# Kernel optimization log

Hardware: AMD Instinct MI355X
Metric: run time of the kernel (lower is better)

## Reference

```python
import jax, jax.numpy as jnp
import numpy as np

HQ, HKV, D = 16, 2, 128   # num_heads_q, num_heads_kv, head_dim
G = HQ // HKV             # q heads per kv head (repeat_interleave factor)


def setup_inputs() -> dict:
    key = jax.random.key(0)
    ks = jax.random.split(key, 6)
    B, T, C = 2, 2048, 2048
    def w(k, shape):
        return jax.random.normal(k, shape, jnp.float32) * (1.0 / np.sqrt(shape[0]).astype(np.float32))
    x = jax.random.normal(ks[0], (B, T, C), jnp.float32)
    Wq = w(ks[1], (C, HQ * D))
    Wk = w(ks[2], (C, HKV * D))
    Wv = w(ks[3], (C, HKV * D))
    Wo = w(ks[4], (HQ * D, C))
    Wg = w(ks[5], (C, HQ))
    # causal mask: True where attention is disallowed (j > i)
    mask = jnp.triu(jnp.ones((T, T), dtype=bool), k=1)[None, None]  # (1,1,T,T)
    return {"x": x, "mask": mask, "Wq": Wq, "Wk": Wk, "Wv": Wv, "Wo": Wo, "Wg": Wg}


def reference(x, mask, Wq, Wk, Wv, Wo, Wg):
    B, T, C = x.shape
    # repeat_interleave(G, dim=heads) means q head h uses kv head h // G,
    # so group q heads as (HKV, G) instead of materializing repeated K/V.
    q = (x @ Wq).reshape(B, T, HKV, G, D).transpose(0, 2, 3, 1, 4)  # (B,HKV,G,T,D)
    k = (x @ Wk).reshape(B, T, HKV, D).transpose(0, 2, 1, 3)        # (B,HKV,T,D)
    v = (x @ Wv).reshape(B, T, HKV, D).transpose(0, 2, 1, 3)        # (B,HKV,T,D)
    scale = jnp.float32(1.0 / np.sqrt(D))
    scores = jnp.einsum('bkgtd,bksd->bkgts', q, k) * scale          # (B,HKV,G,T,T)
    scores = jnp.where(mask[:, None], jnp.float32(-1e9), scores)    # causal fill
    attn = jax.nn.softmax(scores, axis=-1)
    # post-softmax sigmoid gate, one scalar per (batch, q-head, query token)
    gates = jax.nn.sigmoid(x @ Wg)                                   # (B,T,HQ)
    gates = gates.transpose(0, 2, 1).reshape(B, HKV, G, T)           # (B,HKV,G,T)
    out = jnp.einsum('bkgts,bksd->btkgd', attn * gates[..., None], v)
    out = out.reshape(B, T, HQ * D)
    return out @ Wo
```

## Files before the change

### kernel.cpp

```cpp
#include <hip/hip_runtime.h>
#include <hip/hip_bf16.h>
#include <math.h>

#define HQ 16
#define HKV 2
#define D 128
#define B_SZ 2
#define T_SZ 2048
#define C_SZ 2048
#define QKVN 2688

#define C_Q 0.12753102f
#define C_G 1.44269504f

typedef __attribute__((ext_vector_type(8))) short short8;
typedef __attribute__((ext_vector_type(4))) float floatx4;

static __device__ __forceinline__ float fexp2(float x) {
    return __builtin_amdgcn_exp2f(x);
}

static __device__ __forceinline__ unsigned short f2b(float f) {
    union { float f; unsigned u; } x; x.f = f;
    return (unsigned short)((x.u + 0x7fffu + ((x.u >> 16) & 1u)) >> 16);
}

static __device__ __forceinline__ unsigned int pk2(float a, float b) {
    float2 t; t.x = a; t.y = b;
    __hip_bfloat162 h = __float22bfloat162_rn(t);
    return *(unsigned int*)&h;
}

static __device__ __forceinline__ void load_lds16(const void* g, void* l) {
    __builtin_amdgcn_global_load_lds(
        (const __attribute__((address_space(1))) void*)g,
        (__attribute__((address_space(3))) void*)l,
        16, 0, 0);
}

static __device__ __forceinline__ void tr32(
    const float* __restrict__ in, unsigned short* __restrict__ out,
    int R, int Cc, float premul, int bx, int by, float (*t)[33])
{
    const int bc = bx * 32, br = by * 32;
    const int tid = threadIdx.x;
    const int r = tid >> 3, c4 = (tid & 7) * 4;
    float4 v = *(const float4*)(in + (size_t)(br + r) * Cc + bc + c4);
    t[r][c4 + 0] = v.x; t[r][c4 + 1] = v.y; t[r][c4 + 2] = v.z; t[r][c4 + 3] = v.w;
    __syncthreads();
    ushort4 o;
    o.x = f2b(t[c4 + 0][r] * premul); o.y = f2b(t[c4 + 1][r] * premul);
    o.z = f2b(t[c4 + 2][r] * premul); o.w = f2b(t[c4 + 3][r] * premul);
    *(ushort4*)(out + (size_t)(bc + r) * R + br + c4) = o;
}

__global__ __launch_bounds__(256) void prep_kernel(
    const float* __restrict__ x,  const float* __restrict__ Wq,
    const float* __restrict__ Wk, const float* __restrict__ Wv,
    const float* __restrict__ Wo, const float* __restrict__ Wg,
    unsigned short* __restrict__ xb, unsigned short* __restrict__ Wqkvt,
    unsigned short* __restrict__ Wot)
{
    __shared__ float t[32][33];
    const int bid = blockIdx.x;
    const int tid = threadIdx.x;
    if (bid < 4096) {
        int i = bid * 2048 + tid * 8;
        float4 a = *(const float4*)(x + i);
        float4 b = *(const float4*)(x + i + 4);
        ushort4 o0, o1;
        o0.x = f2b(a.x); o0.y = f2b(a.y); o0.z = f2b(a.z); o0.w = f2b(a.w);
        o1.x = f2b(b.x); o1.y = f2b(b.y); o1.z = f2b(b.z); o1.w = f2b(b.w);
        *(ushort4*)(xb + i) = o0;
        *(ushort4*)(xb + i + 4) = o1;
    } else if (bid < 8192) {
        int n = bid - 4096;
        tr32(Wq, Wqkvt, C_SZ, HQ * D, C_Q, n & 63, n >> 6, t);
    } else if (bid < 8704) {
        int n = bid - 8192;
        tr32(Wk, Wqkvt + (size_t)(HQ * D) * C_SZ, C_SZ, HKV * D, 1.0f, n & 7, n >> 3, t);
    } else if (bid < 9216) {
        int n = bid - 8704;
        tr32(Wv, Wqkvt + (size_t)(HQ * D + HKV * D) * C_SZ, C_SZ, HKV * D, 1.0f, n & 7, n >> 3, t);
    } else if (bid < 13312) {
        int n = bid - 9216;
        tr32(Wo, Wot, HQ * D, C_SZ, 1.0f, n & 63, n >> 6, t);
    } else {
        int k = (bid - 13312) * 256 + tid;
        const float4* wr = (const float4*)(Wg + (size_t)k * 16);
        float4 w0 = wr[0], w1 = wr[1], w2 = wr[2], w3 = wr[3];
        float w[16] = {w0.x, w0.y, w0.z, w0.w, w1.x, w1.y, w1.z, w1.w,
                       w2.x, w2.y, w2.z, w2.w, w3.x, w3.y, w3.z, w3.w};
        unsigned short* out = Wqkvt + (size_t)(HQ * D + 2 * HKV * D) * C_SZ;
        #pragma unroll
        for (int h = 0; h < 16; ++h)
            out[(size_t)h * C_SZ + k] = f2b(w[h] * C_G);
    }
}

__global__ __launch_bounds__(256) void gemm_bt_bf16(
    const unsigned short* __restrict__ A, const unsigned short* __restrict__ Bt,
    float* __restrict__ Cf, unsigned short* __restrict__ Cb,
    unsigned short* __restrict__ Vt, int M, int N, int K, int out_bf16)
{
    __shared__ __align__(16) unsigned short SM[8448];
    unsigned short* As = SM;
    unsigned short* Bs = SM + 4096;
    const int tid = threadIdx.x;
    const int lane = tid & 63, wave = tid >> 6;
    const int l15 = lane & 15, quad = lane >> 4;
    const int wr = wave >> 1, wc = wave & 1;
    const int bm = blockIdx.y * 128, bn = blockIdx.x * 128;

    floatx4 zero = {0.f, 0.f, 0.f, 0.f};
    floatx4 acc[4][4];
    #pragma unroll
    for (int i = 0; i < 4; ++i)
        #pragma unroll
        for (int j = 0; j < 4; ++j) acc[i][j] = zero;

    int arow[2], acol[2];
    #pragma unroll
    for (int it = 0; it < 2; ++it) {
        int idx = it * 256 + tid;
        int row = idx >> 2, sb = idx & 3;
        int cb = sb ^ ((row >> 1) & 3);
        arow[it] = row; acol[it] = cb * 8;
    }
    const int sw = quad ^ ((l15 >> 1) & 3);

    for (int k0 = 0; k0 < K; k0 += 32) {
        __syncthreads();
        #pragma unroll
        for (int it = 0; it < 2; ++it) {
            load_lds16(A  + (size_t)(bm + arow[it]) * K + k0 + acol[it],
                       &As[(it * 256 + wave * 64) * 8]);
            load_lds16(Bt + (size_t)(bn + arow[it]) * K + k0 + acol[it],
                       &Bs[(it * 256 + wave * 64) * 8]);
        }
        __syncthreads();

        short8 af[4], bf[4];
        #pragma unroll
        for (int mt = 0; mt < 4; ++mt)
            af[mt] = *(const short8*)&As[((wr * 64 + mt * 16 + l15) * 4 + sw) * 8];
        #pragma unroll
        for (int nt = 0; nt < 4; ++nt)
            bf[nt] = *(const short8*)&Bs[((wc * 64 + nt * 16 + l15) * 4 + sw) * 8];
        #pragma unroll
        for (int mt = 0; mt < 4; ++mt)
            #pragma unroll
            for (int nt = 0; nt < 4; ++nt)
                acc[mt][nt] = __builtin_amdgcn_mfma_f32_16x16x32_bf16(
                    af[mt], bf[nt], acc[mt][nt], 0, 0, 0);
    }

    if (Vt && (bn == 2304 || bn == 2432)) {
        unsigned short (*Ct)[132] = (unsigned short(*)[132])SM;
        const int bb = bm >> 11;
        const int tl = bm & 2047;
        #pragma unroll
        for (int vn = 0; vn < 2; ++vn) {
            __syncthreads();
            if (wc == vn) {
                #pragma unroll
                for (int mt = 0; mt < 4; ++mt)
                    #pragma unroll
                    for (int nt = 0; nt < 4; ++nt)
                        #pragma unroll
                        for (int r = 0; r < 4; ++r)
                            Ct[nt * 16 + l15][wr * 64 + mt * 16 + quad * 4 + r] =
                                f2b(acc[mt][nt][r]);
            }
            __syncthreads();
            int row = tid >> 2, cs = (tid & 3) * 32;
            int vrow = (bn - 2304) + vn * 64 + row;
            unsigned short* dst = Vt + ((size_t)bb * (HKV * D) + vrow) * T_SZ + tl + cs;
            const unsigned short* src = &Ct[row][cs];
            short8 v0 = *(const short8*)(src + 0);
            short8 v1 = *(const short8*)(src + 8);
            short8 v2 = *(const short8*)(src + 16);
            short8 v3 = *(const short8*)(src + 24);
            *(short8*)(dst + 0)  = v0; *(short8*)(dst + 8)  = v1;
            *(short8*)(dst + 16) = v2; *(short8*)(dst + 24) = v3;
        }
        return;
    }

    #pragma unroll
    for (int mt = 0; mt < 4; ++mt)
        #pragma unroll
        for (int nt = 0; nt < 4; ++nt)
            #pragma unroll
            for (int r = 0; r < 4; ++r) {
                int m = bm + wr * 64 + mt * 16 + quad * 4 + r;
                int n = bn + wc * 64 + nt * 16 + l15;
                if (out_bf16) Cb[(size_t)m * N + n] = f2b(acc[mt][nt][r]);
                else          Cf[(size_t)m * N + n] = acc[mt][nt][r];
            }
}

__global__ __launch_bounds__(256) void attn_mfma(
    const unsigned short* __restrict__ QKV, const unsigned short* __restrict__ Vt,
    unsigned short* __restrict__ Ob)
{
    __shared__ __align__(16) unsigned short SMEM[64 * 128 + 128 * 64 + 4 * 16 * 72];
    unsigned short* Ks = SMEM;
    unsigned short* Vs = SMEM + 64 * 128;
    unsigned short* Ps = SMEM + 64 * 128 + 128 * 64;
    unsigned short* Lo = SMEM;

    const int bh = blockIdx.x;
    const int qt = (int)gridDim.y - 1 - (int)blockIdx.y;
    const int b = bh >> 4, h = bh & 15, kvh = h >> 3;
    const int tid = threadIdx.x;
    const int lane = tid & 63, w = tid >> 6;
    const int l15 = lane & 15, quad = lane >> 4;
    const int q_local = w * 16 + l15;
    const float BIAS = 32.0f;

    short8 aq[4];
    {
        const unsigned short* qp = QKV + (size_t)(b * T_SZ + qt * 64 + q_local) * QKVN
                                       + h * D + quad * 8;
        #pragma unroll
        for (int kd = 0; kd < 4; ++kd) aq[kd] = *(const short8*)(qp + kd * 32);
    }

    const unsigned short* kg[4];
    const unsigned short* vg[4];
    #pragma unroll
    for (int it = 0; it < 4; ++it) {
        int Bi = it * 256 + tid;
        int kr = Bi >> 4, kc = ((Bi & 15) ^ (kr & 15)) * 8;
        kg[it] = QKV + (size_t)(b * T_SZ + kr) * QKVN + HQ * D + kvh * D + kc;
        int vr = Bi >> 3, vc = ((Bi & 7) ^ (vr & 7)) * 8;
        vg[it] = Vt + (size_t)((b * HKV + kvh) * D + vr) * T_SZ + vc;
    }

    floatx4 zero = {0.f, 0.f, 0.f, 0.f};
    floatx4 oacc[8];
    #pragma unroll
    for (int dt = 0; dt < 8; ++dt) oacc[dt] = zero;
    float l_part = 0.f;

    for (int kt = 0; kt <= qt; ++kt) {
        __syncthreads();
        #pragma unroll
        for (int it = 0; it < 4; ++it) {
            load_lds16(kg[it] + (size_t)kt * 64 * QKVN, &Ks[(it * 256 + w * 64) * 8]);
            load_lds16(vg[it] + kt * 64,                &Vs[(it * 256 + w * 64) * 8]);
        }
        __syncthreads();

        floatx4 sacc[4];
        #pragma unroll
        for (int nt = 0; nt < 4; ++nt) sacc[nt] = zero;
        #pragma unroll
        for (int kd = 0; kd < 4; ++kd)
            #pragma unroll
            for (int nt = 0; nt < 4; ++nt) {
                short8 ak = *(const short8*)&Ks[((nt * 16 + l15) * 16 + ((kd * 4 + quad) ^ l15)) * 8];
                sacc[nt] = __builtin_amdgcn_mfma_f32_16x16x32_bf16(ak, aq[kd], sacc[nt], 0, 0, 0);
            }

        float p[4][4];
        if (kt == qt) {
            #pragma unroll
            for (int nt = 0; nt < 4; ++nt)
                #pragma unroll
                for (int r = 0; r < 4; ++r) {
                    float e = fexp2(sacc[nt][r] - BIAS);
                    p[nt][r] = (nt * 16 + quad * 4 + r > q_local) ? 0.f : e;
                }
        } else {
            #pragma unroll
            for (int nt = 0; nt < 4; ++nt)
                #pragma unroll
                for (int r = 0; r < 4; ++r)
                    p[nt][r] = fexp2(sacc[nt][r] - BIAS);
        }
        #pragma unroll
        for (int nt = 0; nt < 4; ++nt) {
            l_part += (p[nt][0] + p[nt][1]) + (p[nt][2] + p[nt][3]);
            uint2 pw;
            pw.x = pk2(p[nt][0], p[nt][1]);
            pw.y = pk2(p[nt][2], p[nt][3]);
            *(uint2*)&Ps[(w * 16 + l15) * 72 + nt * 16 + quad * 4] = pw;
        }

        #pragma unroll
        for (int kk = 0; kk < 2; ++kk) {
            short8 bp = *(const short8*)&Ps[(w * 16 + l15) * 72 + kk * 32 + quad * 8];
            #pragma unroll
            for (int dt = 0; dt < 8; ++dt) {
                short8 av = *(const short8*)&Vs[((dt * 16 + l15) * 8 + ((kk * 4 + quad) ^ (l15 & 7))) * 8];
                oacc[dt] = __builtin_amdgcn_mfma_f32_16x16x32_bf16(av, bp, oacc[dt], 0, 0, 0);
            }
        }
    }

    float l = l_part;
    l += __shfl_xor(l, 16);
    l += __shfl_xor(l, 32);

    __syncthreads();
    {
        int token = b * T_SZ + qt * 64 + q_local;
        unsigned short gl = QKV[(size_t)token * QKVN + HQ * D + HKV * D * 2 + h];
        union { unsigned u; float f; } gx; gx.u = ((unsigned)gl) << 16;
        float g = 1.0f / (1.0f + fexp2(-gx.f));
        float f = g / l;
        #pragma unroll
        for (int dt = 0; dt < 8; ++dt) {
            uint2 ov;
            ov.x = pk2(oacc[dt][0] * f, oacc[dt][1] * f);
            ov.y = pk2(oacc[dt][2] * f, oacc[dt][3] * f);
            *(uint2*)&Lo[(size_t)q_local * 136 + dt * 16 + quad * 4] = ov;
        }
    }
    __syncthreads();
    {
        int row = tid >> 2, c0 = (tid & 3) * 32;
        size_t tok = (size_t)(b * T_SZ + qt * 64 + row);
        unsigned short* op = Ob + tok * (HQ * D) + h * D + c0;
        const unsigned short* lp = &Lo[(size_t)row * 136 + c0];
        short8 v0 = *(const short8*)(lp + 0);
        short8 v1 = *(const short8*)(lp + 8);
        short8 v2 = *(const short8*)(lp + 16);
        short8 v3 = *(const short8*)(lp + 24);
        *(short8*)(op + 0)  = v0; *(short8*)(op + 8)  = v1;
        *(short8*)(op + 16) = v2; *(short8*)(op + 24) = v3;
    }
}

extern "C" void kernel_launch(void* const* d_in, const int* in_sizes, int n_in,
                              void* d_out, int out_size, void* d_ws, size_t ws_size,
                              hipStream_t stream) {
    const float* x  = (const float*)d_in[0];
    const float* Wq = (const float*)d_in[2];
    const float* Wk = (const float*)d_in[3];
    const float* Wv = (const float*)d_in[4];
    const float* Wo = (const float*)d_in[5];
    const float* Wg = (const float*)d_in[6];
    float* out = (float*)d_out;

    const size_t KB = 1ull << 10;
    char* p = (char*)d_ws;
    unsigned short* xb    = (unsigned short*)(p);
    unsigned short* Ob    = xb;
    unsigned short* Wqkvt = (unsigned short*)(p + 16384 * KB);
    unsigned short* Wot   = (unsigned short*)(p + 27136 * KB);
    unsigned short* QKV   = (unsigned short*)(p + 35328 * KB);
    unsigned short* Vt    = (unsigned short*)(p + 56832 * KB);
    const int BT = B_SZ * T_SZ;

    prep_kernel<<<dim3(13320), 256, 0, stream>>>(x, Wq, Wk, Wv, Wo, Wg, xb, Wqkvt, Wot);

    gemm_bt_bf16<<<dim3(QKVN / 128, BT / 128), 256, 0, stream>>>(
        xb, Wqkvt, nullptr, QKV, Vt, BT, QKVN, C_SZ, 1);

    attn_mfma<<<dim3(B_SZ * HQ, T_SZ / 64), 256, 0, stream>>>(QKV, Vt, Ob);

    gemm_bt_bf16<<<dim3(C_SZ / 128, BT / 128), 256, 0, stream>>>(
        Ob, Wot, out, nullptr, nullptr, BT, C_SZ, HQ * D, 0);
}
```

Measured before the change: 314.2 us.

## Use 32x32x16 MFMA and 128-query tiles in attention kernel

The attention kernel now processes 128 query rows per block (32 per wave) instead of 64, and switches from 16x16x32 to 32x32x16 bf16 MFMA instructions for both QK^T and PV. Each K/V tile loaded into LDS is therefore reused across twice as many queries, and the larger MFMA reduces LDS fragment reads per flop. The epilogue writes output in two passes through LDS. In exchange, register pressure rises, the grid has half as many blocks, and causal blocks waste more work on masked tiles.

After: 325.2 us. +3.5%, slower.

```diff
diff --git a/kernel.cpp b/kernel.cpp
--- a/kernel.cpp
+++ b/kernel.cpp
@@ -15,6 +15,7 @@
 
 typedef __attribute__((ext_vector_type(8))) short short8;
 typedef __attribute__((ext_vector_type(4))) float floatx4;
+typedef __attribute__((ext_vector_type(16))) float floatx16;
 
 static __device__ __forceinline__ float fexp2(float x) {
     return __builtin_amdgcn_exp2f(x);
@@ -204,10 +205,10 @@
     const unsigned short* __restrict__ QKV, const unsigned short* __restrict__ Vt,
     unsigned short* __restrict__ Ob)
 {
-    __shared__ __align__(16) unsigned short SMEM[64 * 128 + 128 * 64 + 4 * 16 * 72];
+    __shared__ __align__(16) unsigned short SMEM[8192 + 8192 + 4 * 32 * 72];
     unsigned short* Ks = SMEM;
-    unsigned short* Vs = SMEM + 64 * 128;
-    unsigned short* Ps = SMEM + 64 * 128 + 128 * 64;
+    unsigned short* Vs = SMEM + 8192;
+    unsigned short* Ps = SMEM + 16384;
     unsigned short* Lo = SMEM;
 
     const int bh = blockIdx.x;
@@ -215,16 +216,17 @@
     const int b = bh >> 4, h = bh & 15, kvh = h >> 3;
     const int tid = threadIdx.x;
     const int lane = tid & 63, w = tid >> 6;
-    const int l15 = lane & 15, quad = lane >> 4;
-    const int q_local = w * 16 + l15;
+    const int l31 = lane & 31, hi = lane >> 5;
+    const int q_local = w * 32 + l31;
+    const int qglob_l = qt * 128 + q_local;
     const float BIAS = 32.0f;
 
-    short8 aq[4];
+    short8 aq[8];
     {
-        const unsigned short* qp = QKV + (size_t)(b * T_SZ + qt * 64 + q_local) * QKVN
-                                       + h * D + quad * 8;
-        #pragma unroll
-        for (int kd = 0; kd < 4; ++kd) aq[kd] = *(const short8*)(qp + kd * 32);
+        const unsigned short* qp = QKV + (size_t)(b * T_SZ + qglob_l) * QKVN
+                                       + h * D + hi * 8;
+        #pragma unroll
+        for (int kd = 0; kd < 8; ++kd) aq[kd] = *(const short8*)(qp + kd * 16);
     }
 
     const unsigned short* kg[4];
@@ -238,13 +240,15 @@
         vg[it] = Vt + (size_t)((b * HKV + kvh) * D + vr) * T_SZ + vc;
     }
 
-    floatx4 zero = {0.f, 0.f, 0.f, 0.f};
-    floatx4 oacc[8];
-    #pragma unroll
-    for (int dt = 0; dt < 8; ++dt) oacc[dt] = zero;
+    floatx16 oacc[4];
+    #pragma unroll
+    for (int dt2 = 0; dt2 < 4; ++dt2)
+        #pragma unroll
+        for (int r = 0; r < 16; ++r) oacc[dt2][r] = 0.f;
     float l_part = 0.f;
 
-    for (int kt = 0; kt <= qt; ++kt) {
+    const int ktmax = 2 * qt + 1;
+    for (int kt = 0; kt <= ktmax; ++kt) {
         __syncthreads();
         #pragma unroll
         for (int it = 0; it < 4; ++it) {
@@ -253,76 +257,84 @@
         }
         __syncthreads();
 
-        floatx4 sacc[4];
-        #pragma unroll
-        for (int nt = 0; nt < 4; ++nt) sacc[nt] = zero;
-        #pragma unroll
-        for (int kd = 0; kd < 4; ++kd)
-            #pragma unroll
-            for (int nt = 0; nt < 4; ++nt) {
-                short8 ak = *(const short8*)&Ks[((nt * 16 + l15) * 16 + ((kd * 4 + quad) ^ l15)) * 8];
-                sacc[nt] = __builtin_amdgcn_mfma_f32_16x16x32_bf16(ak, aq[kd], sacc[nt], 0, 0, 0);
-            }
-
-        float p[4][4];
-        if (kt == qt) {
-            #pragma unroll
-            for (int nt = 0; nt < 4; ++nt)
+        floatx16 sacc[2];
+        #pragma unroll
+        for (int kt2 = 0; kt2 < 2; ++kt2)
+            #pragma unroll
+            for (int r = 0; r < 16; ++r) sacc[kt2][r] = 0.f;
+        #pragma unroll
+        for (int kd = 0; kd < 8; ++kd)
+            #pragma unroll
+            for (int kt2 = 0; kt2 < 2; ++kt2) {
+                short8 ak = *(const short8*)&Ks[((kt2 * 32 + l31) * 16
+                                + ((kd * 2 + hi) ^ (l31 & 15))) * 8];
+                sacc[kt2] = __builtin_amdgcn_mfma_f32_32x32x16_bf16(
+                    ak, aq[kd], sacc[kt2], 0, 0, 0);
+            }
+
+        #pragma unroll
+        for (int kt2 = 0; kt2 < 2; ++kt2) {
+            float p[16];
+            #pragma unroll
+            for (int r = 0; r < 16; ++r) p[r] = fexp2(sacc[kt2][r] - BIAS);
+            if (kt >= 2 * qt) {
                 #pragma unroll
-                for (int r = 0; r < 4; ++r) {
-                    float e = fexp2(sacc[nt][r] - BIAS);
-                    p[nt][r] = (nt * 16 + quad * 4 + r > q_local) ? 0.f : e;
+                for (int r = 0; r < 16; ++r) {
+                    int key = kt * 64 + kt2 * 32 + (r & 3) + 4 * hi + 8 * (r >> 2);
+                    if (key > qglob_l) p[r] = 0.f;
                 }
-        } else {
-            #pragma unroll
-            for (int nt = 0; nt < 4; ++nt)
+            }
+            #pragma unroll
+            for (int g = 0; g < 4; ++g) {
+                l_part += (p[4 * g] + p[4 * g + 1]) + (p[4 * g + 2] + p[4 * g + 3]);
+                uint2 pw;
+                pw.x = pk2(p[4 * g], p[4 * g + 1]);
+                pw.y = pk2(p[4 * g + 2], p[4 * g + 3]);
+                *(uint2*)&Ps[(w * 32 + l31) * 72 + kt2 * 32 + 8 * g + 4 * hi] = pw;
+            }
+        }
+
+        #pragma unroll
+        for (int kk = 0; kk < 4; ++kk) {
+            short8 bp = *(const short8*)&Ps[(w * 32 + l31) * 72 + kk * 16 + hi * 8];
+            #pragma unroll
+            for (int dt2 = 0; dt2 < 4; ++dt2) {
+                short8 av = *(const short8*)&Vs[((dt2 * 32 + l31) * 8
+                                + ((kk * 2 + hi) ^ (l31 & 7))) * 8];
+                oacc[dt2] = __builtin_amdgcn_mfma_f32_32x32x16_bf16(
+                    av, bp, oacc[dt2], 0, 0, 0);
+            }
+        }
+    }
+
+    float l = l_part + __shfl_xor(l_part, 32);
+
+    float f;
+    {
+        unsigned short gl = QKV[(size_t)(b * T_SZ + qglob_l) * QKVN + HQ * D + 2 * HKV * D + h];
+        union { unsigned u; float ff; } gx; gx.u = ((unsigned)gl) << 16;
+        float g = 1.0f / (1.0f + fexp2(-gx.ff));
+        f = g / l;
+    }
+
+    #pragma unroll
+    for (int pass = 0; pass < 2; ++pass) {
+        __syncthreads();
+        if ((w >> 1) == pass) {
+            int lr = (w & 1) * 32 + l31;
+            #pragma unroll
+            for (int dt2 = 0; dt2 < 4; ++dt2)
                 #pragma unroll
-                for (int r = 0; r < 4; ++r)
-                    p[nt][r] = fexp2(sacc[nt][r] - BIAS);
-        }
-        #pragma unroll
-        for (int nt = 0; nt < 4; ++nt) {
-            l_part += (p[nt][0] + p[nt][1]) + (p[nt][2] + p[nt][3]);
-            uint2 pw;
-            pw.x = pk2(p[nt][0], p[nt][1]);
-            pw.y = pk2(p[nt][2], p[nt][3]);
-            *(uint2*)&Ps[(w * 16 + l15) * 72 + nt * 16 + quad * 4] = pw;
-        }
-
-        #pragma unroll
-        for (int kk = 0; kk < 2; ++kk) {
-            short8 bp = *(const short8*)&Ps[(w * 16 + l15) * 72 + kk * 32 + quad * 8];
-            #pragma unroll
-            for (int dt = 0; dt < 8; ++dt) {
-                short8 av = *(const short8*)&Vs[((dt * 16 + l15) * 8 + ((kk * 4 + quad) ^ (l15 & 7))) * 8];
-                oacc[dt] = __builtin_amdgcn_mfma_f32_16x16x32_bf16(av, bp, oacc[dt], 0, 0, 0);
-            }
-        }
-    }
-
-    float l = l_part;
-    l += __shfl_xor(l, 16);
-    l += __shfl_xor(l, 32);
-
-    __syncthreads();
-    {
-        int token = b * T_SZ + qt * 64 + q_local;
-        unsigned short gl = QKV[(size_t)token * QKVN + HQ * D + HKV * D * 2 + h];
-        union { unsigned u; float f; } gx; gx.u = ((unsigned)gl) << 16;
-        float g = 1.0f / (1.0f + fexp2(-gx.f));
-        float f = g / l;
-        #pragma unroll
-        for (int dt = 0; dt < 8; ++dt) {
-            uint2 ov;
-            ov.x = pk2(oacc[dt][0] * f, oacc[dt][1] * f);
-            ov.y = pk2(oacc[dt][2] * f, oacc[dt][3] * f);
-            *(uint2*)&Lo[(size_t)q_local * 136 + dt * 16 + quad * 4] = ov;
-        }
-    }
-    __syncthreads();
-    {
+                for (int g = 0; g < 4; ++g) {
+                    uint2 ov;
+                    ov.x = pk2(oacc[dt2][4 * g + 0] * f, oacc[dt2][4 * g + 1] * f);
+                    ov.y = pk2(oacc[dt2][4 * g + 2] * f, oacc[dt2][4 * g + 3] * f);
+                    *(uint2*)&Lo[lr * 136 + dt2 * 32 + 8 * g + 4 * hi] = ov;
+                }
+        }
+        __syncthreads();
         int row = tid >> 2, c0 = (tid & 3) * 32;
-        size_t tok = (size_t)(b * T_SZ + qt * 64 + row);
+        size_t tok = (size_t)(b * T_SZ + qt * 128 + pass * 64 + row);
         unsigned short* op = Ob + tok * (HQ * D) + h * D + c0;
         const unsigned short* lp = &Lo[(size_t)row * 136 + c0];
         short8 v0 = *(const short8*)(lp + 0);
@@ -360,7 +372,7 @@
     gemm_bt_bf16<<<dim3(QKVN / 128, BT / 128), 256, 0, stream>>>(
         xb, Wqkvt, nullptr, QKV, Vt, BT, QKVN, C_SZ, 1);
 
-    attn_mfma<<<dim3(B_SZ * HQ, T_SZ / 64), 256, 0, stream>>>(QKV, Vt, Ob);
+    attn_mfma<<<dim3(B_SZ * HQ, T_SZ / 128), 256, 0, stream>>>(QKV, Vt, Ob);
 
     gemm_bt_bf16<<<dim3(C_SZ / 128, BT / 128), 256, 0, stream>>>(
         Ob, Wot, out, nullptr, nullptr, BT, C_SZ, HQ * D, 0);
```
